# Kernel tuning notes

Measured on AMD Instinct MI355X. Metric: run time of the kernel, lower is better.

Reference implementation:

```python
import jax, jax.numpy as jnp
import numpy as np

NEG = -1e9  # matches self.huge in the torch module


def setup_inputs() -> dict:
    key = jax.random.key(0)
    k1, k2, k3 = jax.random.split(key, 3)
    B, n, nt, t = 64, 50, 30, 60
    S = nt + t
    return {
        "unary_scores": jax.random.normal(k1, (B, n, t), dtype=jnp.float32),
        "rule_scores": jax.random.normal(k2, (B, nt, S, S), dtype=jnp.float32),
        "root_scores": jax.random.normal(k3, (B, nt), dtype=jnp.float32),
        "nt_states": nt,
        "t_states": t,
    }


def _inside(unary_scores, rule_scores, root_scores, nt_states, t_states):
    B, n, _ = unary_scores.shape
    S = nt_states + t_states
    # beta chart [B, n+1, n+1, S]. Width-1 cells hold terminal (preterminal)
    # scores at indices [nt:], all other entries are -huge, exactly as in the
    # torch code. Because invalid children are -huge, summing over ALL S
    # child states with the full rule tensor reproduces the original
    # width-2/3/>=4 case split (tmp1/tmp2/tmp3) exactly.
    beta = jnp.full((B, n + 1, n + 1, S), NEG, dtype=unary_scores.dtype)
    ks = jnp.arange(n)
    beta = beta.at[:, ks, ks + 1, nt_states:].set(unary_scores)

    # stabilized exp of rules, shared across all widths (fast-PCFG style)
    m_rule = rule_scores.max(axis=(2, 3))                      # [B, nt]
    erule = jnp.exp(rule_scores - m_rule[:, :, None, None])    # [B, nt, S, S]

    for w in range(2, n + 1):
        ns = n - w + 1                       # number of start positions
        s_idx = jnp.arange(ns)
        u_idx = s_idx[:, None] + jnp.arange(1, w)[None, :]     # [ns, w-1] split points
        lc = beta[:, s_idx[:, None], u_idx, :]                 # [B, ns, k, S]
        rc = beta[:, u_idx, (s_idx + w)[:, None], :]           # [B, ns, k, S]
        m_l = lc.max(-1)                                       # [B, ns, k]
        m_r = rc.max(-1)
        M = (m_l + m_r).max(-1)                                # [B, ns]
        # fold per-split stabilizer into left child
        el = jnp.exp(lc - m_l[..., None]) * jnp.exp(m_l + m_r - M[..., None])[..., None]
        er = jnp.exp(rc - m_r[..., None])
        # logsumexp over (split k, left l, right r) done as two contractions:
        # new[b,n,p] = log sum_{k,l,r} el*er*erule + M + m_rule
        t1 = jnp.einsum('bnkr,bplr->bnkpl', er, erule)         # [B, ns, k, nt, S]
        ssum = jnp.einsum('bnkpl,bnkl->bnp', t1, el)           # [B, ns, nt]
        new = jnp.log(ssum) + M[:, :, None] + m_rule[:, None, :]
        beta = beta.at[:, s_idx, s_idx + w, :nt_states].set(new)

    log_Z = jax.nn.logsumexp(beta[:, 0, n, :nt_states] + root_scores, axis=1)
    return log_Z


def reference(unary_scores, rule_scores, root_scores, nt_states, t_states):
    return _inside(unary_scores, rule_scores, root_scores, int(nt_states), int(t_states))
```

## Files before the change

kernel.cpp:

```cpp
#include <hip/hip_runtime.h>
#include <hip/hip_bf16.h>

#define NEGF (-1000000000.0f)

namespace {

constexpr int B  = 64;
constexpr int N  = 50;
constexpr int NT = 30;
constexpr int T  = 60;
constexpr int S  = 90;
constexpr int NP1 = N + 1;
constexpr int NSMAX = N - 1;
constexpr int SS = S * S;
constexpr int CELLSP = NSMAX * 32 + 32;
constexpr int ECOUNT = B * NP1 * NP1 * S;

constexpr int KP  = 96;
constexpr int KK  = S * KP;
constexpr int KSPL = 15;
constexpr int KT2B = 64;
constexpr int NKT = KK / KT2B;
constexpr int TPC = NKT / KSPL;
constexpr int ROWB  = 72;
constexpr int AOFFB = 32 * ROWB;
constexpr int MTOTB = (32 + 64) * ROWB;

constexpr int S1R = 96;
constexpr int S1STR = 72;

using bf16x8 = __attribute__((ext_vector_type(8))) short;
using f32x4  = __attribute__((ext_vector_type(4))) float;

__device__ __forceinline__ unsigned int pk4_e4m3(float a, float b, float c, float d){
  int w = __builtin_amdgcn_cvt_pk_fp8_f32(a, b, 0, false);
  w = __builtin_amdgcn_cvt_pk_fp8_f32(c, d, w, true);
  return (unsigned int)w;
}

__global__ void unary_init(const float* __restrict__ unary, float* __restrict__ mb,
                           short* __restrict__ E_L, short* __restrict__ E_R){
  int k = blockIdx.x, b = blockIdx.y, j = threadIdx.x;
  float v = (j < T) ? unary[(b*N + k)*T + j] : NEGF;
  float m = v;
  #pragma unroll
  for (int off = 32; off > 0; off >>= 1) m = fmaxf(m, __shfl_xor(m, off));
  if (j == 0) mb[(b*NP1 + k)*NP1 + (k+1)] = m;
  if (j < T){
    __hip_bfloat16 h = __float2bfloat16(__expf(v - m));
    short sv = *reinterpret_cast<short*>(&h);
    E_L[((size_t)((b*NP1 + k)*NP1 + (k+1)))*S + NT + j] = sv;
    E_R[((size_t)((b*NP1 + (k+1))*NP1 + k))*S + NT + j] = sv;
  }
}

__global__ __launch_bounds__(256) void rule_prep(const float* __restrict__ rule,
                                                 float* __restrict__ m_rule,
                                                 unsigned char* __restrict__ erule8){
  int p = blockIdx.x, b = blockIdx.y, tid = threadIdx.x;
  size_t base = (size_t)(b*NT + p) * SS;
  size_t obase = (size_t)(b*NT + p) * KK;
  const float4* r4 = (const float4*)(rule + base);
  float lm = NEGF;
  for (int i = tid; i < SS/4; i += 256){
    float4 v = r4[i];
    lm = fmaxf(fmaxf(lm, fmaxf(v.x, v.y)), fmaxf(v.z, v.w));
  }
  #pragma unroll
  for (int off = 32; off > 0; off >>= 1) lm = fmaxf(lm, __shfl_xor(lm, off));
  __shared__ float wmax[4];
  __shared__ float sm;
  if ((tid & 63) == 0) wmax[tid >> 6] = lm;
  __syncthreads();
  if (tid == 0){
    float m = fmaxf(fmaxf(wmax[0], wmax[1]), fmaxf(wmax[2], wmax[3]));
    m_rule[b*NT + p] = m;
    sm = m;
  }
  __syncthreads();
  float m = sm;
  for (int idx = tid; idx < S * 24; idx += 256){
    int l = idx / 24, q4 = idx - l * 24;
    int r = q4 * 4;
    float e[4];
    #pragma unroll
    for (int j = 0; j < 4; ++j){
      int rr = r + j;
      e[j] = (rr < S) ? __expf(rule[base + l*S + rr] - m) : 0.f;
    }
    *(unsigned int*)&erule8[obase + l*KP + r] = pk4_e4m3(e[0], e[1], e[2], e[3]);
  }
}

__global__ __launch_bounds__(256) void stage1(int w, const short* __restrict__ E_L,
                                              const short* __restrict__ E_R,
                                              const float* __restrict__ mb,
                                              float* __restrict__ Mbuf,
                                              unsigned char* __restrict__ Og8){
  int s = blockIdx.x, b = blockIdx.y, e = s + w, tid = threadIdx.x;
  int K = w - 1;
  int Kpad = (K + 31) & ~31;
  __shared__ float stmp[NSMAX];
  __shared__ float cK[NSMAX];
  __shared__ float sM;
  __shared__ __align__(16) short sbuf[2 * S1R * S1STR];
  short* elT = sbuf;
  short* erT = sbuf + S1R * S1STR;

  if (tid < K){
    int u = s + tid + 1;
    stmp[tid] = mb[(b*NP1 + s)*NP1 + u] + mb[(b*NP1 + u)*NP1 + e];
  }
  __syncthreads();
  if (tid == 0){
    float M = NEGF;
    for (int k = 0; k < K; ++k) M = fmaxf(M, stmp[k]);
    sM = M;
    Mbuf[b*NSMAX + s] = M;
  }
  __syncthreads();
  float M = sM;
  if (tid < K) cK[tid] = __expf(stmp[tid] - M);
  __syncthreads();

  const short* baseL = E_L + ((size_t)((b*NP1 + s)*NP1 + s + 1)) * S;
  const short* baseR = E_R + ((size_t)((b*NP1 + e)*NP1 + s + 1)) * S;

  int items = Kpad * 48;
  for (int idx = tid; idx < items; idx += 256){
    int k = idx / 48, j = idx - k * 48;
    int i = 2 * j;
    short v0 = 0, v1 = 0, r0 = 0, r1 = 0;
    if (k < K && j < 45){
      bool lOK = (k == 0)     ? (j >= 15) : (j < 15);
      bool rOK = (k == K - 1) ? (j >= 15) : (j < 15);
      if (lOK){
        unsigned int L = *(const unsigned int*)(baseL + k*S + i);
        float f0 = __uint_as_float(L << 16) * cK[k];
        float f1 = __uint_as_float(L & 0xFFFF0000u) * cK[k];
        __hip_bfloat16 h0 = __float2bfloat16(f0), h1 = __float2bfloat16(f1);
        v0 = *reinterpret_cast<short*>(&h0);
        v1 = *reinterpret_cast<short*>(&h1);
      }
      if (rOK){
        unsigned int R = *(const unsigned int*)(baseR + k*S + i);
        r0 = (short)(R & 0xFFFFu);
        r1 = (short)(R >> 16);
      }
    }
    elT[i*S1STR + k]     = v0;
    elT[(i+1)*S1STR + k] = v1;
    erT[i*S1STR + k]     = r0;
    erT[(i+1)*S1STR + k] = r1;
  }
  __syncthreads();

  int wid = tid >> 6, lane = tid & 63;
  int rr = lane & 15, hi = lane >> 4;
  int ksteps = Kpad >> 5;
  f32x4 accs[9];
  #pragma unroll
  for (int j = 0; j < 9; ++j){
    int t = wid * 9 + j;
    int tr = t / 6, tc = t - tr * 6;
    int ar = tr*16 + rr, br = tc*16 + rr;
    f32x4 acc = {0.f, 0.f, 0.f, 0.f};
    for (int ks = 0; ks < ksteps; ++ks){
      int kb = ks*32 + hi*8;
      bf16x8 af = *(bf16x8*)&elT[ar*S1STR + kb];
      bf16x8 bf2 = *(bf16x8*)&erT[br*S1STR + kb];
      acc = __builtin_amdgcn_mfma_f32_16x16x32_bf16(af, bf2, acc, 0, 0, 0);
    }
    accs[j] = acc;
  }
  __syncthreads();

  unsigned char* rep = (unsigned char*)sbuf;
  for (int idx = tid; idx < S * (KP - S); idx += 256){
    int l = idx / (KP - S), c = idx - l * (KP - S);
    rep[l*KP + S + c] = 0;
  }
  #pragma unroll
  for (int j = 0; j < 9; ++j){
    int t = wid * 9 + j;
    int tr = t / 6, tc = t - tr * 6;
    int rcol = tc*16 + rr;
    if (rcol < S){
      unsigned int pk = pk4_e4m3(accs[j][0], accs[j][1], accs[j][2], accs[j][3]);
      #pragma unroll
      for (int q = 0; q < 4; ++q){
        int l = tr*16 + hi*4 + q;
        if (l < S) rep[l*KP + rcol] = (unsigned char)((pk >> (8*q)) & 0xff);
      }
    }
  }
  __syncthreads();

  size_t obase = ((size_t)(b*NSMAX + s)) * KK;
  uint4* dst = (uint4*)(Og8 + obase);
  const uint4* src = (const uint4*)rep;
  for (int i = tid; i < KK/16; i += 256) dst[i] = src[i];
}

__global__ __launch_bounds__(512) void stage2(int ns, int ntiles,
                                              const unsigned char* __restrict__ erule8,
                                              const unsigned char* __restrict__ Og8,
                                              float* __restrict__ Cpart){
  int kc = blockIdx.x, b = blockIdx.y, tid = threadIdx.x;
  __shared__ __align__(16) unsigned char ldsb[2 * MTOTB];
  int wid = tid >> 6, lane = tid & 63;
  int mt = wid & 1, nt = wid >> 1;
  f32x4 acc = {0.f, 0.f, 0.f, 0.f};

  for (int i = tid; i < 2*MTOTB/4; i += 512) ((unsigned int*)ldsb)[i] = 0;

  int slot = tid & 7;
  int aRow = (tid >> 3) & 31;
  bool aDo = (tid < 256) && (aRow < NT);
  int bRow = tid >> 3;
  bool bDo = bRow < ns;
  const unsigned char* aSrc = erule8 + ((size_t)(b*NT + (aDo ? aRow : 0))) * KK + slot * 8;
  const unsigned char* bSrc = Og8    + ((size_t)(b*NSMAX + (bDo ? bRow : 0))) * KK + slot * 8;
  int aOff = aRow * ROWB + slot * 8;
  int bOff = AOFFB + bRow * ROWB + slot * 8;

  int arow = mt*16 + (lane & 15);
  int brow = nt*16 + (lane & 15);
  int hi = lane >> 4;
  bool active = nt < ntiles;
  int t0 = kc * TPC;

  uint2 ra, rb;
  if (aDo) ra = *(const uint2*)(aSrc + (size_t)t0 * KT2B);
  if (bDo) rb = *(const uint2*)(bSrc + (size_t)t0 * KT2B);
  __syncthreads();

  int cur = 0;
  for (int tt = 0; tt < TPC; ++tt){
    if (aDo) *(uint2*)&ldsb[cur*MTOTB + aOff] = ra;
    if (bDo) *(uint2*)&ldsb[cur*MTOTB + bOff] = rb;
    if (tt + 1 < TPC){
      size_t koff = (size_t)(t0 + tt + 1) * KT2B;
      if (aDo) ra = *(const uint2*)(aSrc + koff);
      if (bDo) rb = *(const uint2*)(bSrc + koff);
    }
    __syncthreads();
    if (active){
      #pragma unroll
      for (int ks = 0; ks < 2; ++ks){
        int sb = ks*4 + hi;
        long af = *(const long*)&ldsb[cur*MTOTB + arow*ROWB + sb*8];
        long bf2 = *(const long*)&ldsb[cur*MTOTB + AOFFB + brow*ROWB + sb*8];
        acc = __builtin_amdgcn_mfma_f32_16x16x32_fp8_fp8(af, bf2, acc, 0, 0, 0);
      }
    }
    cur ^= 1;
  }

  if (active){
    int scol = nt*16 + (lane & 15);
    if (scol < ns){
      int p0 = mt*16 + hi*4;
      float* cp = Cpart + ((size_t)(kc*B + b)) * CELLSP + scol*32 + p0;
      *(f32x4*)cp = acc;
    }
  }
}

__global__ __launch_bounds__(64) void finalize(int w, const float* __restrict__ Cpart,
                                               const float* __restrict__ Mbuf,
                                               const float* __restrict__ m_rule,
                                               float* __restrict__ mb,
                                               short* __restrict__ E_L,
                                               short* __restrict__ E_R){
  int sp = blockIdx.x, b = blockIdx.y, tid = threadIdx.x;
  __shared__ float qs[32];
  float q = 1e-37f;
  if (tid < NT){
    float sum = 0.f;
    #pragma unroll
    for (int kc = 0; kc < KSPL; ++kc)
      sum += Cpart[((size_t)(kc*B + b))*CELLSP + sp*32 + tid];
    q = sum * __expf(m_rule[b*NT + tid]);
    qs[tid] = q;
  }
  float m = (tid < NT) ? q : 1e-37f;
  #pragma unroll
  for (int off = 32; off > 0; off >>= 1) m = fmaxf(m, __shfl_xor(m, off));
  m = fmaxf(m, 1e-37f);
  __syncthreads();
  if (tid == 0) mb[(b*NP1 + sp)*NP1 + (sp + w)] = Mbuf[b*NSMAX + sp] + __logf(m);
  if (tid < 15){
    float e0 = qs[2*tid] / m, e1 = qs[2*tid + 1] / m;
    __hip_bfloat16 h0 = __float2bfloat16(e0), h1 = __float2bfloat16(e1);
    unsigned int pk = (unsigned int)*(unsigned short*)&h0 |
                      ((unsigned int)*(unsigned short*)&h1 << 16);
    *(unsigned int*)&E_L[((size_t)((b*NP1 + sp)*NP1 + sp + w))*S + 2*tid] = pk;
    *(unsigned int*)&E_R[((size_t)((b*NP1 + sp + w)*NP1 + sp))*S + 2*tid] = pk;
  }
}

__global__ void root_lse(const float* __restrict__ Cpart, const float* __restrict__ Mbuf,
                         const float* __restrict__ m_rule, const float* __restrict__ root,
                         float* __restrict__ out){
  int b = blockIdx.x, j = threadIdx.x;
  float v = NEGF;
  if (j < NT){
    float sum = 0.f;
    #pragma unroll
    for (int q = 0; q < KSPL; ++q)
      sum += Cpart[((size_t)(q*B + b))*CELLSP + j];
    v = __logf(fmaxf(sum, 1e-37f)) + Mbuf[b*NSMAX + 0]
      + m_rule[b*NT + j] + root[b*NT + j];
  }
  float m = v;
  #pragma unroll
  for (int off = 32; off > 0; off >>= 1) m = fmaxf(m, __shfl_xor(m, off));
  float ex = __expf(v - m);
  #pragma unroll
  for (int off = 32; off > 0; off >>= 1) ex += __shfl_xor(ex, off);
  if (j == 0) out[b] = __logf(ex) + m;
}

}

extern "C" void kernel_launch(void* const* d_in, const int* in_sizes, int n_in,
                              void* d_out, int out_size, void* d_ws, size_t ws_size,
                              hipStream_t stream){
  (void)in_sizes; (void)n_in; (void)out_size; (void)ws_size;
  const float* unary = (const float*)d_in[0];
  const float* rule  = (const float*)d_in[1];
  const float* root  = (const float*)d_in[2];

  char* ws = (char*)d_ws;
  size_t off = 0;
  auto alloc = [&](size_t bytes) -> void* {
    void* p = ws + off;
    off += (bytes + 255) & ~(size_t)255;
    return p;
  };
  float* mb     = (float*)alloc(sizeof(float) * (size_t)B * NP1 * NP1);
  float* m_rule = (float*)alloc(sizeof(float) * B * NT);
  float* Mbuf   = (float*)alloc(sizeof(float) * B * NSMAX);
  float* Cpart  = (float*)alloc(sizeof(float) * KSPL * B * CELLSP);
  short* E_L    = (short*)alloc(sizeof(short) * (size_t)ECOUNT);
  short* E_R    = (short*)alloc(sizeof(short) * (size_t)ECOUNT);
  unsigned char* erule8 = (unsigned char*)alloc((size_t)B * NT * KK);
  unsigned char* Og8    = (unsigned char*)alloc((size_t)B * NSMAX * KK);

  unary_init<<<dim3(N, B), dim3(64), 0, stream>>>(unary, mb, E_L, E_R);
  rule_prep<<<dim3(NT, B), dim3(256), 0, stream>>>(rule, m_rule, erule8);

  for (int w = 2; w <= N; ++w){
    int ns = N - w + 1;
    int ntiles = (ns + 15) >> 4;
    stage1<<<dim3(ns, B), dim3(256), 0, stream>>>(w, E_L, E_R, mb, Mbuf, Og8);
    stage2<<<dim3(KSPL, B), dim3(512), 0, stream>>>(ns, ntiles, erule8, Og8, Cpart);
    if (w < N)
      finalize<<<dim3(ns, B), dim3(64), 0, stream>>>(w, Cpart, Mbuf, m_rule, mb, E_L, E_R);
  }
  root_lse<<<dim3(B), dim3(64), 0, stream>>>(Cpart, Mbuf, m_rule, root, (float*)d_out);
}
```

Baseline: 1.543 ms.

## Fold finalize into next-width stage1 to drop a launch per width

Removes the separate finalize kernel. Each stage1 block now reduces the split-K partial sums for its two freshly completed child cells, normalises them, and writes mb and the bf16 E_L/E_R entries. It also feeds those values straight into its own left/right child tiles from shared memory instead of re-reading global memory. Mbuf is double-buffered so the previous width's stabilizers stay readable while the current ones are written. This cuts one launch and one global round-trip per width, at the cost of each block redundantly reducing the Cpart partials for two cells.

```diff
diff --git a/kernel.cpp b/kernel.cpp
--- a/kernel.cpp
+++ b/kernel.cpp
@@ -37,6 +37,10 @@
   w = __builtin_amdgcn_cvt_pk_fp8_f32(c, d, w, true);
   return (unsigned int)w;
 }
+__device__ __forceinline__ short f2bs(float v){
+  __hip_bfloat16 h = __float2bfloat16(v);
+  return *reinterpret_cast<short*>(&h);
+}
 
 __global__ void unary_init(const float* __restrict__ unary, float* __restrict__ mb,
                            short* __restrict__ E_L, short* __restrict__ E_R){
@@ -47,8 +51,7 @@
   for (int off = 32; off > 0; off >>= 1) m = fmaxf(m, __shfl_xor(m, off));
   if (j == 0) mb[(b*NP1 + k)*NP1 + (k+1)] = m;
   if (j < T){
-    __hip_bfloat16 h = __float2bfloat16(__expf(v - m));
-    short sv = *reinterpret_cast<short*>(&h);
+    short sv = f2bs(__expf(v - m));
     E_L[((size_t)((b*NP1 + k)*NP1 + (k+1)))*S + NT + j] = sv;
     E_R[((size_t)((b*NP1 + (k+1))*NP1 + k))*S + NT + j] = sv;
   }
@@ -92,10 +95,14 @@
   }
 }
 
-__global__ __launch_bounds__(256) void stage1(int w, const short* __restrict__ E_L,
-                                              const short* __restrict__ E_R,
-                                              const float* __restrict__ mb,
-                                              float* __restrict__ Mbuf,
+__global__ __launch_bounds__(256) void stage1(int w, int ns,
+                                              const float* __restrict__ Cpart,
+                                              const float* __restrict__ m_rule,
+                                              const float* __restrict__ MbufPrev,
+                                              float* __restrict__ MbufCur,
+                                              short* __restrict__ E_L,
+                                              short* __restrict__ E_R,
+                                              float* __restrict__ mb,
                                               unsigned char* __restrict__ Og8){
   int s = blockIdx.x, b = blockIdx.y, e = s + w, tid = threadIdx.x;
   int K = w - 1;
@@ -103,20 +110,67 @@
   __shared__ float stmp[NSMAX];
   __shared__ float cK[NSMAX];
   __shared__ float sM;
+  __shared__ float qs[2][32];
+  __shared__ float cmax[2];
+  __shared__ float cmb[2];
   __shared__ __align__(16) short sbuf[2 * S1R * S1STR];
   short* elT = sbuf;
   short* erT = sbuf + S1R * S1STR;
 
+  bool hasInline = (w >= 3);
+  if (hasInline){
+    for (int idx = tid; idx < 2*NT; idx += 256){
+      int c = (idx >= NT) ? 1 : 0;
+      int p = idx - c*NT;
+      int sp = s + c;
+      float sum = 0.f;
+      #pragma unroll
+      for (int kc = 0; kc < KSPL; ++kc)
+        sum += Cpart[((size_t)(kc*B + b))*CELLSP + sp*32 + p];
+      qs[c][p] = sum * __expf(m_rule[b*NT + p]);
+    }
+  }
+  __syncthreads();
+  if (hasInline && tid < 2){
+    float m = 1e-37f;
+    for (int p = 0; p < NT; ++p) m = fmaxf(m, qs[tid][p]);
+    cmax[tid] = m;
+    cmb[tid] = MbufPrev[b*NSMAX + (s + tid)] + __logf(m);
+  }
+  __syncthreads();
+
+  if (hasInline){
+    int wp = w - 1;
+    if (tid < 15){
+      float inv = 1.f / cmax[0];
+      unsigned int pk = (unsigned int)(unsigned short)f2bs(qs[0][2*tid] * inv) |
+                        ((unsigned int)(unsigned short)f2bs(qs[0][2*tid+1] * inv) << 16);
+      *(unsigned int*)&E_L[((size_t)((b*NP1 + s)*NP1 + s + wp))*S + 2*tid] = pk;
+      *(unsigned int*)&E_R[((size_t)((b*NP1 + s + wp)*NP1 + s))*S + 2*tid] = pk;
+    } else if (tid >= 32 && tid < 47 && s == ns - 1){
+      int t2 = tid - 32;
+      float inv = 1.f / cmax[1];
+      unsigned int pk = (unsigned int)(unsigned short)f2bs(qs[1][2*t2] * inv) |
+                        ((unsigned int)(unsigned short)f2bs(qs[1][2*t2+1] * inv) << 16);
+      *(unsigned int*)&E_L[((size_t)((b*NP1 + s + 1)*NP1 + s + 1 + wp))*S + 2*t2] = pk;
+      *(unsigned int*)&E_R[((size_t)((b*NP1 + s + 1 + wp)*NP1 + s + 1))*S + 2*t2] = pk;
+    }
+    if (tid == 0) mb[(b*NP1 + s)*NP1 + (s + wp)] = cmb[0];
+    if (tid == 16 && s == ns - 1) mb[(b*NP1 + s + 1)*NP1 + (s + 1 + wp)] = cmb[1];
+  }
+
   if (tid < K){
     int u = s + tid + 1;
-    stmp[tid] = mb[(b*NP1 + s)*NP1 + u] + mb[(b*NP1 + u)*NP1 + e];
+    float ml = (hasInline && tid == K - 1) ? cmb[0] : mb[(b*NP1 + s)*NP1 + u];
+    float mr = (hasInline && tid == 0)     ? cmb[1] : mb[(b*NP1 + u)*NP1 + e];
+    stmp[tid] = ml + mr;
   }
   __syncthreads();
   if (tid == 0){
     float M = NEGF;
     for (int k = 0; k < K; ++k) M = fmaxf(M, stmp[k]);
     sM = M;
-    Mbuf[b*NSMAX + s] = M;
+    MbufCur[b*NSMAX + s] = M;
   }
   __syncthreads();
   float M = sM;
@@ -134,18 +188,31 @@
     if (k < K && j < 45){
       bool lOK = (k == 0)     ? (j >= 15) : (j < 15);
       bool rOK = (k == K - 1) ? (j >= 15) : (j < 15);
+      float ck = cK[k];
       if (lOK){
-        unsigned int L = *(const unsigned int*)(baseL + k*S + i);
-        float f0 = __uint_as_float(L << 16) * cK[k];
-        float f1 = __uint_as_float(L & 0xFFFF0000u) * cK[k];
-        __hip_bfloat16 h0 = __float2bfloat16(f0), h1 = __float2bfloat16(f1);
-        v0 = *reinterpret_cast<short*>(&h0);
-        v1 = *reinterpret_cast<short*>(&h1);
+        float f0, f1;
+        if (hasInline && k == K - 1){
+          float inv = 1.f / cmax[0];
+          f0 = qs[0][i] * inv * ck;
+          f1 = qs[0][i+1] * inv * ck;
+        } else {
+          unsigned int L = *(const unsigned int*)(baseL + k*S + i);
+          f0 = __uint_as_float(L << 16) * ck;
+          f1 = __uint_as_float(L & 0xFFFF0000u) * ck;
+        }
+        v0 = f2bs(f0);
+        v1 = f2bs(f1);
       }
       if (rOK){
-        unsigned int R = *(const unsigned int*)(baseR + k*S + i);
-        r0 = (short)(R & 0xFFFFu);
-        r1 = (short)(R >> 16);
+        if (hasInline && k == 0){
+          float inv = 1.f / cmax[1];
+          r0 = f2bs(qs[1][i] * inv);
+          r1 = f2bs(qs[1][i+1] * inv);
+        } else {
+          unsigned int R = *(const unsigned int*)(baseR + k*S + i);
+          r0 = (short)(R & 0xFFFFu);
+          r1 = (short)(R >> 16);
+        }
       }
     }
     elT[i*S1STR + k]     = v0;
@@ -264,39 +331,6 @@
       float* cp = Cpart + ((size_t)(kc*B + b)) * CELLSP + scol*32 + p0;
       *(f32x4*)cp = acc;
     }
-  }
-}
-
-__global__ __launch_bounds__(64) void finalize(int w, const float* __restrict__ Cpart,
-                                               const float* __restrict__ Mbuf,
-                                               const float* __restrict__ m_rule,
-                                               float* __restrict__ mb,
-                                               short* __restrict__ E_L,
-                                               short* __restrict__ E_R){
-  int sp = blockIdx.x, b = blockIdx.y, tid = threadIdx.x;
-  __shared__ float qs[32];
-  float q = 1e-37f;
-  if (tid < NT){
-    float sum = 0.f;
-    #pragma unroll
-    for (int kc = 0; kc < KSPL; ++kc)
-      sum += Cpart[((size_t)(kc*B + b))*CELLSP + sp*32 + tid];
-    q = sum * __expf(m_rule[b*NT + tid]);
-    qs[tid] = q;
-  }
-  float m = (tid < NT) ? q : 1e-37f;
-  #pragma unroll
-  for (int off = 32; off > 0; off >>= 1) m = fmaxf(m, __shfl_xor(m, off));
-  m = fmaxf(m, 1e-37f);
-  __syncthreads();
-  if (tid == 0) mb[(b*NP1 + sp)*NP1 + (sp + w)] = Mbuf[b*NSMAX + sp] + __logf(m);
-  if (tid < 15){
-    float e0 = qs[2*tid] / m, e1 = qs[2*tid + 1] / m;
-    __hip_bfloat16 h0 = __float2bfloat16(e0), h1 = __float2bfloat16(e1);
-    unsigned int pk = (unsigned int)*(unsigned short*)&h0 |
-                      ((unsigned int)*(unsigned short*)&h1 << 16);
-    *(unsigned int*)&E_L[((size_t)((b*NP1 + sp)*NP1 + sp + w))*S + 2*tid] = pk;
-    *(unsigned int*)&E_R[((size_t)((b*NP1 + sp + w)*NP1 + sp))*S + 2*tid] = pk;
   }
 }
 
@@ -341,7 +375,7 @@
   };
   float* mb     = (float*)alloc(sizeof(float) * (size_t)B * NP1 * NP1);
   float* m_rule = (float*)alloc(sizeof(float) * B * NT);
-  float* Mbuf   = (float*)alloc(sizeof(float) * B * NSMAX);
+  float* Mbuf   = (float*)alloc(sizeof(float) * 2 * B * NSMAX);
   float* Cpart  = (float*)alloc(sizeof(float) * KSPL * B * CELLSP);
   short* E_L    = (short*)alloc(sizeof(short) * (size_t)ECOUNT);
   short* E_R    = (short*)alloc(sizeof(short) * (size_t)ECOUNT);
@@ -354,10 +388,11 @@
   for (int w = 2; w <= N; ++w){
     int ns = N - w + 1;
     int ntiles = (ns + 15) >> 4;
-    stage1<<<dim3(ns, B), dim3(256), 0, stream>>>(w, E_L, E_R, mb, Mbuf, Og8);
+    const float* mprev = Mbuf + ((size_t)((w - 1) & 1)) * B * NSMAX;
+    float*       mcur  = Mbuf + ((size_t)(w & 1)) * B * NSMAX;
+    stage1<<<dim3(ns, B), dim3(256), 0, stream>>>(w, ns, Cpart, m_rule,
+                                                  mprev, mcur, E_L, E_R, mb, Og8);
     stage2<<<dim3(KSPL, B), dim3(512), 0, stream>>>(ns, ntiles, erule8, Og8, Cpart);
-    if (w < N)
-      finalize<<<dim3(ns, B), dim3(64), 0, stream>>>(w, Cpart, Mbuf, m_rule, mb, E_L, E_R);
   }
   root_lse<<<dim3(B), dim3(64), 0, stream>>>(Cpart, Mbuf, m_rule, root, (float*)d_out);
 }
```

New measurement: 1.526 ms. Within noise of the previous version (-1.1%).
